# Kernel tuning notes

Hardware: AMD Instinct MI355X
Metric: run time of the kernel (lower is better)

The kernel has to match this reference:

```python
import jax, jax.numpy as jnp
import numpy as np

SERIES_LEN = 4096
D_EMB = 1024
D_V = 1024
HURST = 0.7
H = HURST - 0.5          # exponent used by the module
DT = 1.0 / SERIES_LEN
EPS = 1e-8


def _attn_matrix():
    # Lower-triangular fractional power-law matrix A2[i, j]:
    #   j <  i : ((i - j) * dt + 1e-8) ** (hurst - 0.5)
    #   j == i : 1e-8 ** (hurst - 0.5)
    #   j >  i : 0
    i = jnp.arange(SERIES_LEN, dtype=jnp.int32)[:, None]
    j = jnp.arange(SERIES_LEN, dtype=jnp.int32)[None, :]
    diff = jnp.clip(i - j, 1, None).astype(jnp.float32)  # safe base for fractional power
    lower = jnp.where(i > j, (diff * DT + EPS) ** H, 0.0)
    diag = jnp.eye(SERIES_LEN, dtype=jnp.float32) * (EPS ** H)
    return lower + diag  # (L, L) float32


def setup_inputs() -> dict:
    key = jax.random.key(0)
    k1, k2 = jax.random.split(key)
    embed_series = jax.random.normal(k1, (D_EMB, SERIES_LEN), dtype=jnp.float32)
    # nn.Linear(d_emb, d_v, bias=False) weight has shape (d_v, d_emb)
    Wv_weight = jax.random.normal(k2, (D_V, D_EMB), dtype=jnp.float32) * (1.0 / np.sqrt(D_EMB))
    return {"embed_series": embed_series, "Wv_weight": Wv_weight}


def reference(embed_series, Wv_weight):
    # V (original, d_v x L) = Wv(embed_series.T).T ; output[i, c] = sum_j A2[i, j] * V[c, j]
    # => out = A2 @ (embed_series.T @ Wv_weight.T), shape (L, d_v)
    A2 = _attn_matrix()                                   # (L, L) lower triangular
    Y = jnp.einsum('el,ve->lv', embed_series, Wv_weight)  # (L, d_v)
    return A2 @ Y                                         # (L, d_v)
```

## Files before the change

### kernel.cpp

```cpp
#include <hip/hip_runtime.h>
#include <hip/hip_bf16.h>
#include <cstdint>
#include <cstddef>


#define L_SER 4096
#define DEMB  1024
#define DV    1024

#define R_STRIDE 4224
#define R_O0     4096
#define LDP      72

typedef __bf16 bf16_t;
typedef __attribute__((ext_vector_type(8))) __bf16 bf16x8;
typedef __attribute__((ext_vector_type(4))) float f32x4;

__global__ void prep_kernel(const float* __restrict__ E, const float* __restrict__ W,
                            bf16_t* __restrict__ Eb, bf16_t* __restrict__ Wb,
                            bf16_t* __restrict__ R) {
    const int b = blockIdx.x;
    if (b < 132) {
        int idx = b * 256 + threadIdx.x;
        int s = idx / R_STRIDE;
        int x = idx - s * R_STRIDE;
        int d = R_O0 + s - x;
        float v = 0.0f;
        if (d >= 0 && d < L_SER)
            v = powf((d == 0) ? 1e-8f : ((float)d * (1.0f / (float)L_SER) + 1e-8f), 0.2f);
        R[idx] = (bf16_t)v;
    } else if (b < 132 + 2048) {
        int idx = (b - 132) * 256 + threadIdx.x;
        const f32x4* s = (const f32x4*)E;
        f32x4 v0 = s[idx * 2], v1 = s[idx * 2 + 1];
        bf16x8 o;
        o[0] = (bf16_t)v0[0]; o[1] = (bf16_t)v0[1]; o[2] = (bf16_t)v0[2]; o[3] = (bf16_t)v0[3];
        o[4] = (bf16_t)v1[0]; o[5] = (bf16_t)v1[1]; o[6] = (bf16_t)v1[2]; o[7] = (bf16_t)v1[3];
        ((bf16x8*)Eb)[idx] = o;
    } else {
        int idx = (b - 2180) * 256 + threadIdx.x;
        const f32x4* s = (const f32x4*)W;
        f32x4 v0 = s[idx * 2], v1 = s[idx * 2 + 1];
        bf16x8 o;
        o[0] = (bf16_t)v0[0]; o[1] = (bf16_t)v0[1]; o[2] = (bf16_t)v0[2]; o[3] = (bf16_t)v0[3];
        o[4] = (bf16_t)v1[0]; o[5] = (bf16_t)v1[1]; o[6] = (bf16_t)v1[2]; o[7] = (bf16_t)v1[3];
        ((bf16x8*)Wb)[idx] = o;
    }
}

#define GA_STAGE(SBOFS, RA, RB)                                              \
    _Pragma("unroll")                                                        \
    for (int c = 0; c < 4; ++c) {                                            \
        *(bf16x8*)&sA[(SBOFS) + (c * 32 + srow) * LDP + kc8] = RA[c];        \
        *(bf16x8*)&sB[(SBOFS) + (c * 32 + srow) * LDP + kc8] = RB[c];        \
    }

#define GA_PREFETCH(RA, RB)                                                  \
    _Pragma("unroll")                                                        \
    for (int c = 0; c < 4; ++c) {                                            \
        RA[c] = *(const bf16x8*)pA[c];                                       \
        RB[c] = *(const bf16x8*)pB[c];                                       \
        pA[c] += 64; pB[c] += 64;                                            \
    }

#define GA_COMPUTE(SBOFS)                                                    \
    _Pragma("unroll")                                                        \
    for (int kk = 0; kk < 2; ++kk) {                                         \
        bf16x8 afr[4], bfr[4];                                               \
        _Pragma("unroll")                                                    \
        for (int tm = 0; tm < 4; ++tm)                                       \
            afr[tm] = *(const bf16x8*)&sA[(SBOFS) + (wm * 64 + tm * 16 + ln) * LDP + kk * 32 + quad * 8]; \
        _Pragma("unroll")                                                    \
        for (int tn = 0; tn < 4; ++tn)                                       \
            bfr[tn] = *(const bf16x8*)&sB[(SBOFS) + (wn * 64 + tn * 16 + ln) * LDP + kk * 32 + quad * 8]; \
        _Pragma("unroll")                                                    \
        for (int tm = 0; tm < 4; ++tm)                                       \
            _Pragma("unroll")                                                \
            for (int tn = 0; tn < 4; ++tn)                                   \
                acc[tm][tn] = __builtin_amdgcn_mfma_f32_16x16x32_bf16(afr[tm], bfr[tn], acc[tm][tn], 0, 0, 0); \
    }

__global__ __launch_bounds__(256, 2) void gemm_a_kernel(const bf16_t* __restrict__ R,
                                                        const bf16_t* __restrict__ Eb,
                                                        bf16_t* __restrict__ T0,
                                                        bf16_t* __restrict__ T1) {
    __shared__ __align__(16) bf16_t sA[2 * 128 * LDP];
    __shared__ __align__(16) bf16_t sB[2 * 128 * LDP];

    const int bid = blockIdx.x;
    int I, nb, h;
    if (bid < 256) { I = bid >> 3;                nb = bid & 7;         h = 0; }
    else           { I = 31 - ((bid - 256) >> 3); nb = (bid - 256) & 7; h = 1; }
    const int i0 = I * 128;
    const int n0 = nb * 128;
    const int nsteps = I + 1;
    const int j0b = h ? 64 * (I + 1) : 0;
    bf16_t* __restrict__ Tout = h ? T1 : T0;

    const int tid  = threadIdx.x;
    const int wave = tid >> 6;
    const int lane = tid & 63;
    const int quad = lane >> 4;
    const int ln   = lane & 15;
    const int wm   = wave >> 1;
    const int wn   = wave & 1;
    const int srow = tid >> 3;
    const int kc8  = (tid & 7) * 8;

    f32x4 acc[4][4];
#pragma unroll
    for (int a = 0; a < 4; ++a)
#pragma unroll
        for (int b = 0; b < 4; ++b) acc[a][b] = (f32x4){0, 0, 0, 0};

    const bf16_t* pA[4];
    const bf16_t* pB[4];
    bf16x8 ra0[4], rb0[4], ra1[4], rb1[4];
#pragma unroll
    for (int c = 0; c < 4; ++c) {
        int r = c * 32 + srow;
        pA[c] = R + (size_t)(r & 7) * R_STRIDE + (R_O0 - i0 + j0b - 8 * (r >> 3) + kc8);
        pB[c] = Eb + (size_t)(n0 + c * 32 + srow) * L_SER + j0b + kc8;
    }
    GA_PREFETCH(ra0, rb0)
    if (nsteps > 1) { GA_PREFETCH(ra1, rb1) }

    for (int s = 0;; s += 2) {
        GA_STAGE(0, ra0, rb0)
        __syncthreads();
        if (s + 2 < nsteps) { GA_PREFETCH(ra0, rb0) }
        GA_COMPUTE(0)
        if (s + 1 >= nsteps) break;
        GA_STAGE(128 * LDP, ra1, rb1)
        __syncthreads();
        if (s + 3 < nsteps) { GA_PREFETCH(ra1, rb1) }
        GA_COMPUTE(128 * LDP)
        if (s + 2 >= nsteps) break;
    }

#pragma unroll
    for (int tm = 0; tm < 4; ++tm) {
        int row_base = i0 + wm * 64 + tm * 16 + quad * 4;
#pragma unroll
        for (int tn = 0; tn < 4; ++tn) {
            int col = n0 + wn * 64 + tn * 16 + ln;
#pragma unroll
            for (int r = 0; r < 4; ++r)
                Tout[(size_t)(row_base + r) * DEMB + col] = (bf16_t)acc[tm][tn][r];
        }
    }
}

#define GB_STAGE(SBOFS_A, SBOFS_B, RA, RB)                                   \
    _Pragma("unroll")                                                        \
    for (int c = 0; c < 2; ++c)                                              \
        *(bf16x8*)&sA[(SBOFS_A) + (c * 32 + srow) * LDP + kc8] = RA[c];      \
    _Pragma("unroll")                                                        \
    for (int c = 0; c < 4; ++c)                                              \
        *(bf16x8*)&sB[(SBOFS_B) + (c * 32 + srow) * LDP + kc8] = RB[c];

#define GB_PREFETCH(RA, RB)                                                  \
    _Pragma("unroll")                                                        \
    for (int c = 0; c < 2; ++c) {                                            \
        bf16x8 t0 = *(const bf16x8*)p0[c];                                   \
        bf16x8 t1 = *(const bf16x8*)p1[c];                                   \
        bf16x8 o;                                                            \
        _Pragma("unroll")                                                    \
        for (int u = 0; u < 8; ++u) o[u] = (bf16_t)((float)t0[u] + (float)t1[u]); \
        RA[c] = o;                                                           \
        p0[c] += 64; p1[c] += 64;                                            \
    }                                                                        \
    _Pragma("unroll")                                                        \
    for (int c = 0; c < 4; ++c) {                                            \
        RB[c] = *(const bf16x8*)pW[c];                                       \
        pW[c] += 64;                                                         \
    }

#define GB_COMPUTE(SBOFS_A, SBOFS_B)                                         \
    _Pragma("unroll")                                                        \
    for (int kk = 0; kk < 2; ++kk) {                                         \
        bf16x8 afr[2], bfr[4];                                               \
        _Pragma("unroll")                                                    \
        for (int tm = 0; tm < 2; ++tm)                                       \
            afr[tm] = *(const bf16x8*)&sA[(SBOFS_A) + (wm * 32 + tm * 16 + ln) * LDP + kk * 32 + quad * 8]; \
        _Pragma("unroll")                                                    \
        for (int tn = 0; tn < 4; ++tn)                                       \
            bfr[tn] = *(const bf16x8*)&sB[(SBOFS_B) + (wn * 64 + tn * 16 + ln) * LDP + kk * 32 + quad * 8]; \
        _Pragma("unroll")                                                    \
        for (int tm = 0; tm < 2; ++tm)                                       \
            _Pragma("unroll")                                                \
            for (int tn = 0; tn < 4; ++tn)                                   \
                acc[tm][tn] = __builtin_amdgcn_mfma_f32_16x16x32_bf16(afr[tm], bfr[tn], acc[tm][tn], 0, 0, 0); \
    }

__global__ __launch_bounds__(256, 2) void gemm_b_kernel(const bf16_t* __restrict__ T0,
                                                        const bf16_t* __restrict__ T1,
                                                        const bf16_t* __restrict__ Wb,
                                                        float* __restrict__ out) {
    __shared__ __align__(16) bf16_t sA[2 * 64 * LDP];
    __shared__ __align__(16) bf16_t sB[2 * 128 * LDP];

    const int bid = blockIdx.x;
    const int ib = bid >> 3;
    const int nb = bid & 7;
    const int i0 = ib * 64;
    const int n0 = nb * 128;

    const int tid  = threadIdx.x;
    const int wave = tid >> 6;
    const int lane = tid & 63;
    const int quad = lane >> 4;
    const int ln   = lane & 15;
    const int wm   = wave >> 1;
    const int wn   = wave & 1;
    const int srow = tid >> 3;
    const int kc8  = (tid & 7) * 8;

    f32x4 acc[2][4];
#pragma unroll
    for (int a = 0; a < 2; ++a)
#pragma unroll
        for (int b = 0; b < 4; ++b) acc[a][b] = (f32x4){0, 0, 0, 0};

    const int nsteps = DEMB / 64;

    const bf16_t* p0[2];
    const bf16_t* p1[2];
    const bf16_t* pW[4];
    bf16x8 ra0[2], rb0[4], ra1[2], rb1[4];
#pragma unroll
    for (int c = 0; c < 2; ++c) {
        size_t arow = (size_t)(i0 + c * 32 + srow) * DEMB + kc8;
        p0[c] = T0 + arow;
        p1[c] = T1 + arow;
    }
#pragma unroll
    for (int c = 0; c < 4; ++c)
        pW[c] = Wb + (size_t)(n0 + c * 32 + srow) * DEMB + kc8;

    GB_PREFETCH(ra0, rb0)
    GB_PREFETCH(ra1, rb1)

    for (int s = 0;; s += 2) {
        GB_STAGE(0, 0, ra0, rb0)
        __syncthreads();
        if (s + 2 < nsteps) { GB_PREFETCH(ra0, rb0) }
        GB_COMPUTE(0, 0)
        GB_STAGE(64 * LDP, 128 * LDP, ra1, rb1)
        __syncthreads();
        if (s + 3 < nsteps) { GB_PREFETCH(ra1, rb1) }
        GB_COMPUTE(64 * LDP, 128 * LDP)
        if (s + 2 >= nsteps) break;
    }

#pragma unroll
    for (int tm = 0; tm < 2; ++tm) {
        int row_base = i0 + wm * 32 + tm * 16 + quad * 4;
#pragma unroll
        for (int tn = 0; tn < 4; ++tn) {
            int col = n0 + wn * 64 + tn * 16 + ln;
#pragma unroll
            for (int r = 0; r < 4; ++r)
                out[(size_t)(row_base + r) * DV + col] = acc[tm][tn][r];
        }
    }
}

extern "C" void kernel_launch(void* const* d_in, const int* in_sizes, int n_in,
                              void* d_out, int out_size, void* d_ws, size_t ws_size,
                              hipStream_t stream) {
    const float* E = (const float*)d_in[0];
    const float* W = (const float*)d_in[1];
    float* out = (float*)d_out;

    char* ws = (char*)d_ws;
    bf16_t* Eb = (bf16_t*)(ws);
    bf16_t* T0 = (bf16_t*)(ws + (size_t)8  * 1024 * 1024);
    bf16_t* T1 = (bf16_t*)(ws + (size_t)16 * 1024 * 1024);
    bf16_t* Wb = (bf16_t*)(ws + (size_t)24 * 1024 * 1024);
    bf16_t* R  = (bf16_t*)(ws + (size_t)26 * 1024 * 1024);

    prep_kernel<<<2692, 256, 0, stream>>>(E, W, Eb, Wb, R);
    gemm_a_kernel<<<512, 256, 0, stream>>>(R, Eb, T0, T1);
    gemm_b_kernel<<<512, 256, 0, stream>>>(T0, T1, Wb, out);
}
```

Before: 133.2 us.

## Drop LDS staging: load MFMA fragments directly from global, add separate T-sum kernel

Both GEMM kernels stop staging tiles through shared memory with barriers. Each wave now loads its MFMA fragments straight from global memory (the Toeplitz R table and Eb, or Ts and Wb) into double-buffered registers. The Toeplitz table stride is widened so the per-lane shifted reads stay in bounds. The T0+T1 sum moves out of gemm_b's prefetch into a separate elementwise kernel. This removes LDS traffic and syncs, but it loses cross-wave reuse, so global/L2 traffic rises and uncoalesced row-strided loads plus an extra launch are added.

```diff
diff --git a/kernel.cpp b/kernel.cpp
--- a/kernel.cpp
+++ b/kernel.cpp
@@ -8,9 +8,9 @@
 #define DEMB  1024
 #define DV    1024
 
-#define R_STRIDE 4224
+#define R_STRIDE 4288
+#define R_TOT    (8 * R_STRIDE)
 #define R_O0     4096
-#define LDP      72
 
 typedef __bf16 bf16_t;
 typedef __attribute__((ext_vector_type(8))) __bf16 bf16x8;
@@ -20,7 +20,7 @@
                             bf16_t* __restrict__ Eb, bf16_t* __restrict__ Wb,
                             bf16_t* __restrict__ R) {
     const int b = blockIdx.x;
-    if (b < 132) {
+    if (b < 134) {
         int idx = b * 256 + threadIdx.x;
         int s = idx / R_STRIDE;
         int x = idx - s * R_STRIDE;
@@ -29,8 +29,8 @@
         if (d >= 0 && d < L_SER)
             v = powf((d == 0) ? 1e-8f : ((float)d * (1.0f / (float)L_SER) + 1e-8f), 0.2f);
         R[idx] = (bf16_t)v;
-    } else if (b < 132 + 2048) {
-        int idx = (b - 132) * 256 + threadIdx.x;
+    } else if (b < 134 + 2048) {
+        int idx = (b - 134) * 256 + threadIdx.x;
         const f32x4* s = (const f32x4*)E;
         f32x4 v0 = s[idx * 2], v1 = s[idx * 2 + 1];
         bf16x8 o;
@@ -38,7 +38,7 @@
         o[4] = (bf16_t)v1[0]; o[5] = (bf16_t)v1[1]; o[6] = (bf16_t)v1[2]; o[7] = (bf16_t)v1[3];
         ((bf16x8*)Eb)[idx] = o;
     } else {
-        int idx = (b - 2180) * 256 + threadIdx.x;
+        int idx = (b - 2182) * 256 + threadIdx.x;
         const f32x4* s = (const f32x4*)W;
         f32x4 v0 = s[idx * 2], v1 = s[idx * 2 + 1];
         bf16x8 o;
@@ -48,45 +48,46 @@
     }
 }
 
-#define GA_STAGE(SBOFS, RA, RB)                                              \
-    _Pragma("unroll")                                                        \
-    for (int c = 0; c < 4; ++c) {                                            \
-        *(bf16x8*)&sA[(SBOFS) + (c * 32 + srow) * LDP + kc8] = RA[c];        \
-        *(bf16x8*)&sB[(SBOFS) + (c * 32 + srow) * LDP + kc8] = RB[c];        \
-    }
-
-#define GA_PREFETCH(RA, RB)                                                  \
-    _Pragma("unroll")                                                        \
-    for (int c = 0; c < 4; ++c) {                                            \
-        RA[c] = *(const bf16x8*)pA[c];                                       \
-        RB[c] = *(const bf16x8*)pB[c];                                       \
-        pA[c] += 64; pB[c] += 64;                                            \
-    }
-
-#define GA_COMPUTE(SBOFS)                                                    \
-    _Pragma("unroll")                                                        \
-    for (int kk = 0; kk < 2; ++kk) {                                         \
-        bf16x8 afr[4], bfr[4];                                               \
-        _Pragma("unroll")                                                    \
-        for (int tm = 0; tm < 4; ++tm)                                       \
-            afr[tm] = *(const bf16x8*)&sA[(SBOFS) + (wm * 64 + tm * 16 + ln) * LDP + kk * 32 + quad * 8]; \
-        _Pragma("unroll")                                                    \
-        for (int tn = 0; tn < 4; ++tn)                                       \
-            bfr[tn] = *(const bf16x8*)&sB[(SBOFS) + (wn * 64 + tn * 16 + ln) * LDP + kk * 32 + quad * 8]; \
-        _Pragma("unroll")                                                    \
-        for (int tm = 0; tm < 4; ++tm)                                       \
-            _Pragma("unroll")                                                \
-            for (int tn = 0; tn < 4; ++tn)                                   \
-                acc[tm][tn] = __builtin_amdgcn_mfma_f32_16x16x32_bf16(afr[tm], bfr[tn], acc[tm][tn], 0, 0, 0); \
-    }
+__global__ void tsum_kernel(const bf16_t* __restrict__ T0, const bf16_t* __restrict__ T1,
+                            bf16_t* __restrict__ Ts) {
+    int idx = blockIdx.x * blockDim.x + threadIdx.x;
+    bf16x8 a = ((const bf16x8*)T0)[idx];
+    bf16x8 b = ((const bf16x8*)T1)[idx];
+    bf16x8 o;
+#pragma unroll
+    for (int u = 0; u < 8; ++u) o[u] = (bf16_t)((float)a[u] + (float)b[u]);
+    ((bf16x8*)Ts)[idx] = o;
+}
+
+#define GA_LOAD(AF, BF, PA, PB)                                               \
+    _Pragma("unroll")                                                         \
+    for (int tm = 0; tm < 4; ++tm)                                            \
+        _Pragma("unroll")                                                     \
+        for (int kk = 0; kk < 2; ++kk)                                        \
+            AF[tm * 2 + kk] = *(const bf16x8*)((PA) - 16 * tm + 32 * kk);     \
+    (PA) += 128;                                                              \
+    _Pragma("unroll")                                                         \
+    for (int tn = 0; tn < 4; ++tn) {                                          \
+        _Pragma("unroll")                                                     \
+        for (int kk = 0; kk < 2; ++kk)                                        \
+            BF[tn * 2 + kk] = *(const bf16x8*)((PB)[tn] + 32 * kk);           \
+        (PB)[tn] += 128;                                                      \
+    }
+
+#define GA_MFMA(AF, BF)                                                       \
+    _Pragma("unroll")                                                         \
+    for (int kk = 0; kk < 2; ++kk)                                            \
+        _Pragma("unroll")                                                     \
+        for (int tm = 0; tm < 4; ++tm)                                        \
+            _Pragma("unroll")                                                 \
+            for (int tn = 0; tn < 4; ++tn)                                    \
+                acc[tm][tn] = __builtin_amdgcn_mfma_f32_16x16x32_bf16(        \
+                    AF[tm * 2 + kk], BF[tn * 2 + kk], acc[tm][tn], 0, 0, 0);
 
 __global__ __launch_bounds__(256, 2) void gemm_a_kernel(const bf16_t* __restrict__ R,
                                                         const bf16_t* __restrict__ Eb,
                                                         bf16_t* __restrict__ T0,
                                                         bf16_t* __restrict__ T1) {
-    __shared__ __align__(16) bf16_t sA[2 * 128 * LDP];
-    __shared__ __align__(16) bf16_t sB[2 * 128 * LDP];
-
     const int bid = blockIdx.x;
     int I, nb, h;
     if (bid < 256) { I = bid >> 3;                nb = bid & 7;         h = 0; }
@@ -104,8 +105,6 @@
     const int ln   = lane & 15;
     const int wm   = wave >> 1;
     const int wn   = wave & 1;
-    const int srow = tid >> 3;
-    const int kc8  = (tid & 7) * 8;
 
     f32x4 acc[4][4];
 #pragma unroll
@@ -113,28 +112,29 @@
 #pragma unroll
         for (int b = 0; b < 4; ++b) acc[a][b] = (f32x4){0, 0, 0, 0};
 
-    const bf16_t* pA[4];
-    const bf16_t* pB[4];
-    bf16x8 ra0[4], rb0[4], ra1[4], rb1[4];
-#pragma unroll
-    for (int c = 0; c < 4; ++c) {
-        int r = c * 32 + srow;
-        pA[c] = R + (size_t)(r & 7) * R_STRIDE + (R_O0 - i0 + j0b - 8 * (r >> 3) + kc8);
-        pB[c] = Eb + (size_t)(n0 + c * 32 + srow) * L_SER + j0b + kc8;
-    }
-    GA_PREFETCH(ra0, rb0)
-    if (nsteps > 1) { GA_PREFETCH(ra1, rb1) }
+    const int s_rep = ln & 7;
+    const bf16_t* paBase = R + (size_t)s_rep * R_STRIDE
+                         + (R_O0 + s_rep - (i0 + wm * 64 + ln) + quad * 8);
+    const bf16_t* pa0 = paBase + j0b;
+    const bf16_t* pa1 = paBase + j0b + 64;
+    const bf16_t* pb0[4];
+    const bf16_t* pb1[4];
+#pragma unroll
+    for (int tn = 0; tn < 4; ++tn) {
+        pb0[tn] = Eb + (size_t)(n0 + wn * 64 + tn * 16 + ln) * L_SER + j0b + quad * 8;
+        pb1[tn] = pb0[tn] + 64;
+    }
+
+    bf16x8 afr0[8], bfr0[8], afr1[8], bfr1[8];
+    GA_LOAD(afr0, bfr0, pa0, pb0)
+    if (nsteps > 1) { GA_LOAD(afr1, bfr1, pa1, pb1) }
 
     for (int s = 0;; s += 2) {
-        GA_STAGE(0, ra0, rb0)
-        __syncthreads();
-        if (s + 2 < nsteps) { GA_PREFETCH(ra0, rb0) }
-        GA_COMPUTE(0)
+        GA_MFMA(afr0, bfr0)
+        if (s + 2 < nsteps) { GA_LOAD(afr0, bfr0, pa0, pb0) }
         if (s + 1 >= nsteps) break;
-        GA_STAGE(128 * LDP, ra1, rb1)
-        __syncthreads();
-        if (s + 3 < nsteps) { GA_PREFETCH(ra1, rb1) }
-        GA_COMPUTE(128 * LDP)
+        GA_MFMA(afr1, bfr1)
+        if (s + 3 < nsteps) { GA_LOAD(afr1, bfr1, pa1, pb1) }
         if (s + 2 >= nsteps) break;
     }
 
@@ -151,55 +151,35 @@
     }
 }
 
-#define GB_STAGE(SBOFS_A, SBOFS_B, RA, RB)                                   \
-    _Pragma("unroll")                                                        \
-    for (int c = 0; c < 2; ++c)                                              \
-        *(bf16x8*)&sA[(SBOFS_A) + (c * 32 + srow) * LDP + kc8] = RA[c];      \
-    _Pragma("unroll")                                                        \
-    for (int c = 0; c < 4; ++c)                                              \
-        *(bf16x8*)&sB[(SBOFS_B) + (c * 32 + srow) * LDP + kc8] = RB[c];
-
-#define GB_PREFETCH(RA, RB)                                                  \
-    _Pragma("unroll")                                                        \
-    for (int c = 0; c < 2; ++c) {                                            \
-        bf16x8 t0 = *(const bf16x8*)p0[c];                                   \
-        bf16x8 t1 = *(const bf16x8*)p1[c];                                   \
-        bf16x8 o;                                                            \
-        _Pragma("unroll")                                                    \
-        for (int u = 0; u < 8; ++u) o[u] = (bf16_t)((float)t0[u] + (float)t1[u]); \
-        RA[c] = o;                                                           \
-        p0[c] += 64; p1[c] += 64;                                            \
-    }                                                                        \
-    _Pragma("unroll")                                                        \
-    for (int c = 0; c < 4; ++c) {                                            \
-        RB[c] = *(const bf16x8*)pW[c];                                       \
-        pW[c] += 64;                                                         \
-    }
-
-#define GB_COMPUTE(SBOFS_A, SBOFS_B)                                         \
-    _Pragma("unroll")                                                        \
-    for (int kk = 0; kk < 2; ++kk) {                                         \
-        bf16x8 afr[2], bfr[4];                                               \
-        _Pragma("unroll")                                                    \
-        for (int tm = 0; tm < 2; ++tm)                                       \
-            afr[tm] = *(const bf16x8*)&sA[(SBOFS_A) + (wm * 32 + tm * 16 + ln) * LDP + kk * 32 + quad * 8]; \
-        _Pragma("unroll")                                                    \
-        for (int tn = 0; tn < 4; ++tn)                                       \
-            bfr[tn] = *(const bf16x8*)&sB[(SBOFS_B) + (wn * 64 + tn * 16 + ln) * LDP + kk * 32 + quad * 8]; \
-        _Pragma("unroll")                                                    \
-        for (int tm = 0; tm < 2; ++tm)                                       \
-            _Pragma("unroll")                                                \
-            for (int tn = 0; tn < 4; ++tn)                                   \
-                acc[tm][tn] = __builtin_amdgcn_mfma_f32_16x16x32_bf16(afr[tm], bfr[tn], acc[tm][tn], 0, 0, 0); \
-    }
-
-__global__ __launch_bounds__(256, 2) void gemm_b_kernel(const bf16_t* __restrict__ T0,
-                                                        const bf16_t* __restrict__ T1,
+#define GB_LOAD(AF, BF, PA, PB)                                               \
+    _Pragma("unroll")                                                         \
+    for (int tm = 0; tm < 2; ++tm) {                                          \
+        _Pragma("unroll")                                                     \
+        for (int kk = 0; kk < 2; ++kk)                                        \
+            AF[tm * 2 + kk] = *(const bf16x8*)((PA)[tm] + 32 * kk);           \
+        (PA)[tm] += 128;                                                      \
+    }                                                                         \
+    _Pragma("unroll")                                                         \
+    for (int tn = 0; tn < 4; ++tn) {                                          \
+        _Pragma("unroll")                                                     \
+        for (int kk = 0; kk < 2; ++kk)                                        \
+            BF[tn * 2 + kk] = *(const bf16x8*)((PB)[tn] + 32 * kk);           \
+        (PB)[tn] += 128;                                                      \
+    }
+
+#define GB_MFMA(AF, BF)                                                       \
+    _Pragma("unroll")                                                         \
+    for (int kk = 0; kk < 2; ++kk)                                            \
+        _Pragma("unroll")                                                     \
+        for (int tm = 0; tm < 2; ++tm)                                        \
+            _Pragma("unroll")                                                 \
+            for (int tn = 0; tn < 4; ++tn)                                    \
+                acc[tm][tn] = __builtin_amdgcn_mfma_f32_16x16x32_bf16(        \
+                    AF[tm * 2 + kk], BF[tn * 2 + kk], acc[tm][tn], 0, 0, 0);
+
+__global__ __launch_bounds__(256, 2) void gemm_b_kernel(const bf16_t* __restrict__ Ts,
                                                         const bf16_t* __restrict__ Wb,
                                                         float* __restrict__ out) {
-    __shared__ __align__(16) bf16_t sA[2 * 64 * LDP];
-    __shared__ __align__(16) bf16_t sB[2 * 128 * LDP];
-
     const int bid = blockIdx.x;
     const int ib = bid >> 3;
     const int nb = bid & 7;
@@ -213,8 +193,6 @@
     const int ln   = lane & 15;
     const int wm   = wave >> 1;
     const int wn   = wave & 1;
-    const int srow = tid >> 3;
-    const int kc8  = (tid & 7) * 8;
 
     f32x4 acc[2][4];
 #pragma unroll
@@ -224,32 +202,30 @@
 
     const int nsteps = DEMB / 64;
 
-    const bf16_t* p0[2];
-    const bf16_t* p1[2];
-    const bf16_t* pW[4];
-    bf16x8 ra0[2], rb0[4], ra1[2], rb1[4];
-#pragma unroll
-    for (int c = 0; c < 2; ++c) {
-        size_t arow = (size_t)(i0 + c * 32 + srow) * DEMB + kc8;
-        p0[c] = T0 + arow;
-        p1[c] = T1 + arow;
-    }
-#pragma unroll
-    for (int c = 0; c < 4; ++c)
-        pW[c] = Wb + (size_t)(n0 + c * 32 + srow) * DEMB + kc8;
-
-    GB_PREFETCH(ra0, rb0)
-    GB_PREFETCH(ra1, rb1)
+    const bf16_t* pa0[2];
+    const bf16_t* pa1[2];
+    const bf16_t* pb0[4];
+    const bf16_t* pb1[4];
+#pragma unroll
+    for (int tm = 0; tm < 2; ++tm) {
+        pa0[tm] = Ts + (size_t)(i0 + wm * 32 + tm * 16 + ln) * DEMB + quad * 8;
+        pa1[tm] = pa0[tm] + 64;
+    }
+#pragma unroll
+    for (int tn = 0; tn < 4; ++tn) {
+        pb0[tn] = Wb + (size_t)(n0 + wn * 64 + tn * 16 + ln) * DEMB + quad * 8;
+        pb1[tn] = pb0[tn] + 64;
+    }
+
+    bf16x8 afr0[4], bfr0[8], afr1[4], bfr1[8];
+    GB_LOAD(afr0, bfr0, pa0, pb0)
+    GB_LOAD(afr1, bfr1, pa1, pb1)
 
     for (int s = 0;; s += 2) {
-        GB_STAGE(0, 0, ra0, rb0)
-        __syncthreads();
-        if (s + 2 < nsteps) { GB_PREFETCH(ra0, rb0) }
-        GB_COMPUTE(0, 0)
-        GB_STAGE(64 * LDP, 128 * LDP, ra1, rb1)
-        __syncthreads();
-        if (s + 3 < nsteps) { GB_PREFETCH(ra1, rb1) }
-        GB_COMPUTE(64 * LDP, 128 * LDP)
+        GB_MFMA(afr0, bfr0)
+        if (s + 2 < nsteps) { GB_LOAD(afr0, bfr0, pa0, pb0) }
+        GB_MFMA(afr1, bfr1)
+        if (s + 3 < nsteps) { GB_LOAD(afr1, bfr1, pa1, pb1) }
         if (s + 2 >= nsteps) break;
     }
 
@@ -277,10 +253,12 @@
     bf16_t* Eb = (bf16_t*)(ws);
     bf16_t* T0 = (bf16_t*)(ws + (size_t)8  * 1024 * 1024);
     bf16_t* T1 = (bf16_t*)(ws + (size_t)16 * 1024 * 1024);
-    bf16_t* Wb = (bf16_t*)(ws + (size_t)24 * 1024 * 1024);
-    bf16_t* R  = (bf16_t*)(ws + (size_t)26 * 1024 * 1024);
-
-    prep_kernel<<<2692, 256, 0, stream>>>(E, W, Eb, Wb, R);
+    bf16_t* Tsm= (bf16_t*)(ws + (size_t)24 * 1024 * 1024);
+    bf16_t* Wb = (bf16_t*)(ws + (size_t)32 * 1024 * 1024);
+    bf16_t* R  = (bf16_t*)(ws + (size_t)34 * 1024 * 1024);
+
+    prep_kernel<<<2694, 256, 0, stream>>>(E, W, Eb, Wb, R);
     gemm_a_kernel<<<512, 256, 0, stream>>>(R, Eb, T0, T1);
-    gemm_b_kernel<<<512, 256, 0, stream>>>(T0, T1, Wb, out);
-}
+    tsum_kernel<<<2048, 256, 0, stream>>>(T0, T1, Tsm);
+    gemm_b_kernel<<<512, 256, 0, stream>>>(Tsm, Wb, out);
+}
```

New measurement: 226.9 us. 1.7x slower.

## Split causal GEMM K-range four ways and stage tiles via direct global-to-LDS loads

Applied to the files above, without the earlier changes.

The first GEMM now splits each row block's causal K-range into four balanced partial sums, launching twice as many blocks, and writes four partial buffers. Its tiles are loaded with global_load_lds directly into unpadded LDS in a single-buffered loop, replacing the register-staged double buffer. The second GEMM sums four partials on load and uses smaller 64x64 tiles with higher occupancy. This trades extra partial-buffer traffic and possible LDS bank conflicts from the unpadded layout for better load balance and more parallelism.

```diff
diff --git a/kernel.cpp b/kernel.cpp
--- a/kernel.cpp
+++ b/kernel.cpp
@@ -8,19 +8,26 @@
 #define DEMB  1024
 #define DV    1024
 
-#define R_STRIDE 4224
+#define R_STRIDE 4288
+#define R_TOT    (8 * R_STRIDE)
 #define R_O0     4096
 #define LDP      72
 
 typedef __bf16 bf16_t;
 typedef __attribute__((ext_vector_type(8))) __bf16 bf16x8;
 typedef __attribute__((ext_vector_type(4))) float f32x4;
+
+__device__ __forceinline__ void load_lds16(const void* g, void* l) {
+    __builtin_amdgcn_global_load_lds(
+        (const __attribute__((address_space(1))) void*)g,
+        (__attribute__((address_space(3))) void*)l, 16, 0, 0);
+}
 
 __global__ void prep_kernel(const float* __restrict__ E, const float* __restrict__ W,
                             bf16_t* __restrict__ Eb, bf16_t* __restrict__ Wb,
                             bf16_t* __restrict__ R) {
     const int b = blockIdx.x;
-    if (b < 132) {
+    if (b < 134) {
         int idx = b * 256 + threadIdx.x;
         int s = idx / R_STRIDE;
         int x = idx - s * R_STRIDE;
@@ -29,8 +36,8 @@
         if (d >= 0 && d < L_SER)
             v = powf((d == 0) ? 1e-8f : ((float)d * (1.0f / (float)L_SER) + 1e-8f), 0.2f);
         R[idx] = (bf16_t)v;
-    } else if (b < 132 + 2048) {
-        int idx = (b - 132) * 256 + threadIdx.x;
+    } else if (b < 134 + 2048) {
+        int idx = (b - 134) * 256 + threadIdx.x;
         const f32x4* s = (const f32x4*)E;
         f32x4 v0 = s[idx * 2], v1 = s[idx * 2 + 1];
         bf16x8 o;
@@ -38,7 +45,7 @@
         o[4] = (bf16_t)v1[0]; o[5] = (bf16_t)v1[1]; o[6] = (bf16_t)v1[2]; o[7] = (bf16_t)v1[3];
         ((bf16x8*)Eb)[idx] = o;
     } else {
-        int idx = (b - 2180) * 256 + threadIdx.x;
+        int idx = (b - 2182) * 256 + threadIdx.x;
         const f32x4* s = (const f32x4*)W;
         f32x4 v0 = s[idx * 2], v1 = s[idx * 2 + 1];
         bf16x8 o;
@@ -48,54 +55,27 @@
     }
 }
 
-#define GA_STAGE(SBOFS, RA, RB)                                              \
-    _Pragma("unroll")                                                        \
-    for (int c = 0; c < 4; ++c) {                                            \
-        *(bf16x8*)&sA[(SBOFS) + (c * 32 + srow) * LDP + kc8] = RA[c];        \
-        *(bf16x8*)&sB[(SBOFS) + (c * 32 + srow) * LDP + kc8] = RB[c];        \
-    }
-
-#define GA_PREFETCH(RA, RB)                                                  \
-    _Pragma("unroll")                                                        \
-    for (int c = 0; c < 4; ++c) {                                            \
-        RA[c] = *(const bf16x8*)pA[c];                                       \
-        RB[c] = *(const bf16x8*)pB[c];                                       \
-        pA[c] += 64; pB[c] += 64;                                            \
-    }
-
-#define GA_COMPUTE(SBOFS)                                                    \
-    _Pragma("unroll")                                                        \
-    for (int kk = 0; kk < 2; ++kk) {                                         \
-        bf16x8 afr[4], bfr[4];                                               \
-        _Pragma("unroll")                                                    \
-        for (int tm = 0; tm < 4; ++tm)                                       \
-            afr[tm] = *(const bf16x8*)&sA[(SBOFS) + (wm * 64 + tm * 16 + ln) * LDP + kk * 32 + quad * 8]; \
-        _Pragma("unroll")                                                    \
-        for (int tn = 0; tn < 4; ++tn)                                       \
-            bfr[tn] = *(const bf16x8*)&sB[(SBOFS) + (wn * 64 + tn * 16 + ln) * LDP + kk * 32 + quad * 8]; \
-        _Pragma("unroll")                                                    \
-        for (int tm = 0; tm < 4; ++tm)                                       \
-            _Pragma("unroll")                                                \
-            for (int tn = 0; tn < 4; ++tn)                                   \
-                acc[tm][tn] = __builtin_amdgcn_mfma_f32_16x16x32_bf16(afr[tm], bfr[tn], acc[tm][tn], 0, 0, 0); \
-    }
-
-__global__ __launch_bounds__(256, 2) void gemm_a_kernel(const bf16_t* __restrict__ R,
-                                                        const bf16_t* __restrict__ Eb,
-                                                        bf16_t* __restrict__ T0,
-                                                        bf16_t* __restrict__ T1) {
-    __shared__ __align__(16) bf16_t sA[2 * 128 * LDP];
-    __shared__ __align__(16) bf16_t sB[2 * 128 * LDP];
+__global__ __launch_bounds__(256) void gemm_a_kernel(const bf16_t* __restrict__ R,
+                                                     const bf16_t* __restrict__ Eb,
+                                                     bf16_t* __restrict__ T0,
+                                                     bf16_t* __restrict__ T1,
+                                                     bf16_t* __restrict__ T2,
+                                                     bf16_t* __restrict__ T3) {
+    __shared__ __align__(16) bf16_t sA[128 * 64];
+    __shared__ __align__(16) bf16_t sB[128 * 64];
 
     const int bid = blockIdx.x;
-    int I, nb, h;
-    if (bid < 256) { I = bid >> 3;                nb = bid & 7;         h = 0; }
-    else           { I = 31 - ((bid - 256) >> 3); nb = (bid - 256) & 7; h = 1; }
+    const int I   = 31 - (bid >> 5);
+    const int sub = bid & 31;
+    const int q   = sub >> 3;
+    const int nb  = sub & 7;
     const int i0 = I * 128;
     const int n0 = nb * 128;
-    const int nsteps = I + 1;
-    const int j0b = h ? 64 * (I + 1) : 0;
-    bf16_t* __restrict__ Tout = h ? T1 : T0;
+    const int tot  = 2 * (I + 1);
+    const int base = tot >> 2, rem = tot & 3;
+    const int nsteps = base + (q < rem ? 1 : 0);
+    const int j0b = 64 * (q * base + (q < rem ? q : rem));
+    bf16_t* __restrict__ Tout = (q == 0) ? T0 : (q == 1) ? T1 : (q == 2) ? T2 : T3;
 
     const int tid  = threadIdx.x;
     const int wave = tid >> 6;
@@ -115,27 +95,42 @@
 
     const bf16_t* pA[4];
     const bf16_t* pB[4];
-    bf16x8 ra0[4], rb0[4], ra1[4], rb1[4];
 #pragma unroll
     for (int c = 0; c < 4; ++c) {
         int r = c * 32 + srow;
         pA[c] = R + (size_t)(r & 7) * R_STRIDE + (R_O0 - i0 + j0b - 8 * (r >> 3) + kc8);
         pB[c] = Eb + (size_t)(n0 + c * 32 + srow) * L_SER + j0b + kc8;
     }
-    GA_PREFETCH(ra0, rb0)
-    if (nsteps > 1) { GA_PREFETCH(ra1, rb1) }
-
-    for (int s = 0;; s += 2) {
-        GA_STAGE(0, ra0, rb0)
-        __syncthreads();
-        if (s + 2 < nsteps) { GA_PREFETCH(ra0, rb0) }
-        GA_COMPUTE(0)
-        if (s + 1 >= nsteps) break;
-        GA_STAGE(128 * LDP, ra1, rb1)
-        __syncthreads();
-        if (s + 3 < nsteps) { GA_PREFETCH(ra1, rb1) }
-        GA_COMPUTE(128 * LDP)
-        if (s + 2 >= nsteps) break;
+
+    for (int s = 0; s < nsteps; ++s) {
+#pragma unroll
+        for (int c = 0; c < 4; ++c) {
+            load_lds16(pA[c], &sA[c * 2048 + tid * 8]);
+            pA[c] += 64;
+        }
+#pragma unroll
+        for (int c = 0; c < 4; ++c) {
+            load_lds16(pB[c], &sB[c * 2048 + tid * 8]);
+            pB[c] += 64;
+        }
+        __syncthreads();
+
+#pragma unroll
+        for (int kk = 0; kk < 2; ++kk) {
+            bf16x8 afr[4], bfr[4];
+#pragma unroll
+            for (int tm = 0; tm < 4; ++tm)
+                afr[tm] = *(const bf16x8*)&sA[(wm * 64 + tm * 16 + ln) * 64 + kk * 32 + quad * 8];
+#pragma unroll
+            for (int tn = 0; tn < 4; ++tn)
+                bfr[tn] = *(const bf16x8*)&sB[(wn * 64 + tn * 16 + ln) * 64 + kk * 32 + quad * 8];
+#pragma unroll
+            for (int tm = 0; tm < 4; ++tm)
+#pragma unroll
+                for (int tn = 0; tn < 4; ++tn)
+                    acc[tm][tn] = __builtin_amdgcn_mfma_f32_16x16x32_bf16(afr[tm], bfr[tn], acc[tm][tn], 0, 0, 0);
+        }
+        __syncthreads();
     }
 
 #pragma unroll
@@ -151,60 +146,65 @@
     }
 }
 
-#define GB_STAGE(SBOFS_A, SBOFS_B, RA, RB)                                   \
-    _Pragma("unroll")                                                        \
-    for (int c = 0; c < 2; ++c)                                              \
-        *(bf16x8*)&sA[(SBOFS_A) + (c * 32 + srow) * LDP + kc8] = RA[c];      \
-    _Pragma("unroll")                                                        \
-    for (int c = 0; c < 4; ++c)                                              \
-        *(bf16x8*)&sB[(SBOFS_B) + (c * 32 + srow) * LDP + kc8] = RB[c];
+#define GB_STAGE(SBOFS, RA, RB)                                              \
+    _Pragma("unroll")                                                        \
+    for (int c = 0; c < 2; ++c) {                                            \
+        *(bf16x8*)&sA[(SBOFS) + (c * 32 + srow) * LDP + kc8] = RA[c];        \
+        *(bf16x8*)&sB[(SBOFS) + (c * 32 + srow) * LDP + kc8] = RB[c];        \
+    }
 
 #define GB_PREFETCH(RA, RB)                                                  \
     _Pragma("unroll")                                                        \
     for (int c = 0; c < 2; ++c) {                                            \
         bf16x8 t0 = *(const bf16x8*)p0[c];                                   \
         bf16x8 t1 = *(const bf16x8*)p1[c];                                   \
+        bf16x8 t2 = *(const bf16x8*)p2[c];                                   \
+        bf16x8 t3 = *(const bf16x8*)p3[c];                                   \
         bf16x8 o;                                                            \
         _Pragma("unroll")                                                    \
-        for (int u = 0; u < 8; ++u) o[u] = (bf16_t)((float)t0[u] + (float)t1[u]); \
+        for (int u = 0; u < 8; ++u)                                          \
+            o[u] = (bf16_t)(((float)t0[u] + (float)t1[u]) +                  \
+                            ((float)t2[u] + (float)t3[u]));                  \
         RA[c] = o;                                                           \
-        p0[c] += 64; p1[c] += 64;                                            \
+        p0[c] += 64; p1[c] += 64; p2[c] += 64; p3[c] += 64;                  \
     }                                                                        \
     _Pragma("unroll")                                                        \
-    for (int c = 0; c < 4; ++c) {                                            \
+    for (int c = 0; c < 2; ++c) {                                            \
         RB[c] = *(const bf16x8*)pW[c];                                       \
         pW[c] += 64;                                                         \
     }
 
-#define GB_COMPUTE(SBOFS_A, SBOFS_B)                                         \
+#define GB_COMPUTE(SBOFS)                                                    \
     _Pragma("unroll")                                                        \
     for (int kk = 0; kk < 2; ++kk) {                                         \
-        bf16x8 afr[2], bfr[4];                                               \
+        bf16x8 afr[2], bfr[2];                                               \
         _Pragma("unroll")                                                    \
         for (int tm = 0; tm < 2; ++tm)                                       \
-            afr[tm] = *(const bf16x8*)&sA[(SBOFS_A) + (wm * 32 + tm * 16 + ln) * LDP + kk * 32 + quad * 8]; \
-        _Pragma("unroll")                                                    \
-        for (int tn = 0; tn < 4; ++tn)                                       \
-            bfr[tn] = *(const bf16x8*)&sB[(SBOFS_B) + (wn * 64 + tn * 16 + ln) * LDP + kk * 32 + quad * 8]; \
+            afr[tm] = *(const bf16x8*)&sA[(SBOFS) + (wm * 32 + tm * 16 + ln) * LDP + kk * 32 + quad * 8]; \
+        _Pragma("unroll")                                                    \
+        for (int tn = 0; tn < 2; ++tn)                                       \
+            bfr[tn] = *(const bf16x8*)&sB[(SBOFS) + (wn * 32 + tn * 16 + ln) * LDP + kk * 32 + quad * 8]; \
         _Pragma("unroll")                                                    \
         for (int tm = 0; tm < 2; ++tm)                                       \
             _Pragma("unroll")                                                \
-            for (int tn = 0; tn < 4; ++tn)                                   \
+            for (int tn = 0; tn < 2; ++tn)                                   \
                 acc[tm][tn] = __builtin_amdgcn_mfma_f32_16x16x32_bf16(afr[tm], bfr[tn], acc[tm][tn], 0, 0, 0); \
     }
 
-__global__ __launch_bounds__(256, 2) void gemm_b_kernel(const bf16_t* __restrict__ T0,
+__global__ __launch_bounds__(256, 4) void gemm_b_kernel(const bf16_t* __restrict__ T0,
                                                         const bf16_t* __restrict__ T1,
+                                                        const bf16_t* __restrict__ T2,
+                                                        const bf16_t* __restrict__ T3,
                                                         const bf16_t* __restrict__ Wb,
                                                         float* __restrict__ out) {
     __shared__ __align__(16) bf16_t sA[2 * 64 * LDP];
-    __shared__ __align__(16) bf16_t sB[2 * 128 * LDP];
+    __shared__ __align__(16) bf16_t sB[2 * 64 * LDP];
 
     const int bid = blockIdx.x;
-    const int ib = bid >> 3;
-    const int nb = bid & 7;
+    const int ib = bid >> 4;
+    const int nb = bid & 15;
     const int i0 = ib * 64;
-    const int n0 = nb * 128;
+    const int n0 = nb * 64;
 
     const int tid  = threadIdx.x;
     const int wave = tid >> 6;
@@ -216,40 +216,42 @@
     const int srow = tid >> 3;
     const int kc8  = (tid & 7) * 8;
 
-    f32x4 acc[2][4];
+    f32x4 acc[2][2];
 #pragma unroll
     for (int a = 0; a < 2; ++a)
 #pragma unroll
-        for (int b = 0; b < 4; ++b) acc[a][b] = (f32x4){0, 0, 0, 0};
+        for (int b = 0; b < 2; ++b) acc[a][b] = (f32x4){0, 0, 0, 0};
 
     const int nsteps = DEMB / 64;
 
     const bf16_t* p0[2];
     const bf16_t* p1[2];
-    const bf16_t* pW[4];
-    bf16x8 ra0[2], rb0[4], ra1[2], rb1[4];
+    const bf16_t* p2[2];
+    const bf16_t* p3[2];
+    const bf16_t* pW[2];
+    bf16x8 ra0[2], rb0[2], ra1[2], rb1[2];
 #pragma unroll
     for (int c = 0; c < 2; ++c) {
         size_t arow = (size_t)(i0 + c * 32 + srow) * DEMB + kc8;
         p0[c] = T0 + arow;
         p1[c] = T1 + arow;
-    }
-#pragma unroll
-    for (int c = 0; c < 4; ++c)
+        p2[c] = T2 + arow;
+        p3[c] = T3 + arow;
         pW[c] = Wb + (size_t)(n0 + c * 32 + srow) * DEMB + kc8;
+    }
 
     GB_PREFETCH(ra0, rb0)
     GB_PREFETCH(ra1, rb1)
 
     for (int s = 0;; s += 2) {
-        GB_STAGE(0, 0, ra0, rb0)
+        GB_STAGE(0, ra0, rb0)
         __syncthreads();
         if (s + 2 < nsteps) { GB_PREFETCH(ra0, rb0) }
-        GB_COMPUTE(0, 0)
-        GB_STAGE(64 * LDP, 128 * LDP, ra1, rb1)
+        GB_COMPUTE(0)
+        GB_STAGE(64 * LDP, ra1, rb1)
         __syncthreads();
         if (s + 3 < nsteps) { GB_PREFETCH(ra1, rb1) }
-        GB_COMPUTE(64 * LDP, 128 * LDP)
+        GB_COMPUTE(64 * LDP)
         if (s + 2 >= nsteps) break;
     }
 
@@ -257,8 +259,8 @@
     for (int tm = 0; tm < 2; ++tm) {
         int row_base = i0 + wm * 32 + tm * 16 + quad * 4;
 #pragma unroll
-        for (int tn = 0; tn < 4; ++tn) {
-            int col = n0 + wn * 64 + tn * 16 + ln;
+        for (int tn = 0; tn < 2; ++tn) {
+            int col = n0 + wn * 32 + tn * 16 + ln;
 #pragma unroll
             for (int r = 0; r < 4; ++r)
                 out[(size_t)(row_base + r) * DV + col] = acc[tm][tn][r];
@@ -277,10 +279,12 @@
     bf16_t* Eb = (bf16_t*)(ws);
     bf16_t* T0 = (bf16_t*)(ws + (size_t)8  * 1024 * 1024);
     bf16_t* T1 = (bf16_t*)(ws + (size_t)16 * 1024 * 1024);
-    bf16_t* Wb = (bf16_t*)(ws + (size_t)24 * 1024 * 1024);
-    bf16_t* R  = (bf16_t*)(ws + (size_t)26 * 1024 * 1024);
-
-    prep_kernel<<<2692, 256, 0, stream>>>(E, W, Eb, Wb, R);
-    gemm_a_kernel<<<512, 256, 0, stream>>>(R, Eb, T0, T1);
-    gemm_b_kernel<<<512, 256, 0, stream>>>(T0, T1, Wb, out);
-}
+    bf16_t* T2 = (bf16_t*)(ws + (size_t)24 * 1024 * 1024);
+    bf16_t* T3 = (bf16_t*)(ws + (size_t)32 * 1024 * 1024);
+    bf16_t* Wb = (bf16_t*)(ws + (size_t)40 * 1024 * 1024);
+    bf16_t* R  = (bf16_t*)(ws + (size_t)42 * 1024 * 1024);
+
+    prep_kernel<<<2694, 256, 0, stream>>>(E, W, Eb, Wb, R);
+    gemm_a_kernel<<<1024, 256, 0, stream>>>(R, Eb, T0, T1, T2, T3);
+    gemm_b_kernel<<<1024, 256, 0, stream>>>(T0, T1, T2, T3, Wb, out);
+}
```

Result: slower. 145.3 us (+9.1%).
